# Kernel optimization log

Measured on AMD Instinct MI355X. Metric: run time of the kernel, lower is better.

The kernel has to match this reference:

```python
import jax, jax.numpy as jnp
import numpy as np

B, N, H, HD = 2, 512, 1024, 512


def setup_inputs() -> dict:
    key = jax.random.key(0)
    ks = jax.random.split(key, 9)
    s = 0.02
    return {
        "emb": jax.random.normal(ks[0], (B, N, H), jnp.float32),
        # start detector: Linear(H->HD), ReLU, Linear(HD->1)
        "W_s1": jax.random.normal(ks[1], (H, HD), jnp.float32) * s,
        "b_s1": jax.random.normal(ks[2], (HD,), jnp.float32) * s,
        "w_s2": jax.random.normal(ks[3], (HD,), jnp.float32) * s,
        "b_s2": jax.random.normal(ks[4], (), jnp.float32) * s,
        # end detector: Linear(2H->HD), ReLU, Linear(HD->1)
        "W_e1": jax.random.normal(ks[5], (2 * H, HD), jnp.float32) * s,
        "b_e1": jax.random.normal(ks[6], (HD,), jnp.float32) * s,
        "w_e2": jax.random.normal(ks[7], (HD,), jnp.float32) * s,
        "b_e2": jax.random.normal(ks[8], (), jnp.float32) * s,
    }


def reference(emb, W_s1, b_s1, w_s2, b_s2, W_e1, b_e1, w_e2, b_e2):
    # start logits: (B, N)
    h_s = jax.nn.relu(jnp.einsum("bnh,hd->bnd", emb, W_s1) + b_s1)
    start_logits = jnp.einsum("bnd,d->bn", h_s, w_s2) + b_s2

    # end logits: math of cat([start_rep, end_rep]) @ W_e1 done as split matmuls
    # (avoids materializing the (B,N,N,2H) concat buffer)
    W1_start, W1_end = W_e1[:H], W_e1[H:]
    a = jnp.einsum("bih,hd->bid", emb, W1_start)  # (B, N, HD) start-token part
    c = jnp.einsum("bjh,hd->bjd", emb, W1_end)    # (B, N, HD) end-token part
    h_e = jax.nn.relu(a[:, :, None, :] + c[:, None, :, :] + b_e1)  # (B, N, N, HD)
    end_logits = jnp.einsum("bijd,d->bij", h_e, w_e2) + b_e2       # (B, N, N)

    return (start_logits, end_logits)
```

## Files before the change

### kernel.cpp

```cpp
#include <hip/hip_runtime.h>
#include <hip/hip_bf16.h>


typedef float f32x4 __attribute__((ext_vector_type(4)));
typedef float f32x2 __attribute__((ext_vector_type(2)));
typedef __bf16 bf16x8 __attribute__((ext_vector_type(8)));

static __device__ __forceinline__ unsigned short f2bf(float f) {
  unsigned int u = __builtin_bit_cast(unsigned int, f);
  u += 0x7FFFu + ((u >> 16) & 1u);
  return (unsigned short)(u >> 16);
}

__global__ __launch_bounds__(256) void prep(
    const float* __restrict__ emb, const float* __restrict__ W_s1,
    const float* __restrict__ W_e1, const float* __restrict__ b_s2,
    unsigned short* __restrict__ emb_bf, unsigned short* __restrict__ Wt_s,
    unsigned short* __restrict__ Wt_e, float* __restrict__ out) {
  __shared__ float tile[32][33];
  int bx = blockIdx.x, t = threadIdx.x;
  if (bx < 512) {
    int i = bx * 2048 + t * 8;
    f32x4 v0 = *(const f32x4*)&emb[i];
    f32x4 v1 = *(const f32x4*)&emb[i + 4];
    ushort4 o0, o1;
    o0.x = f2bf(v0[0]); o0.y = f2bf(v0[1]);
    o0.z = f2bf(v0[2]); o0.w = f2bf(v0[3]);
    o1.x = f2bf(v1[0]); o1.y = f2bf(v1[1]);
    o1.z = f2bf(v1[2]); o1.w = f2bf(v1[3]);
    *(ushort4*)&emb_bf[i] = o0;
    *(ushort4*)&emb_bf[i + 4] = o1;
  } else if (bx < 2048) {
    const float* in;
    unsigned short* o;
    int R, tid;
    if (bx < 1024) { tid = bx - 512;  in = W_s1; o = Wt_s; R = 1024; }
    else           { tid = bx - 1024; in = W_e1; o = Wt_e; R = 2048; }
    int r0 = (tid >> 4) * 32, c0 = (tid & 15) * 32;
    int a = t >> 3, b4 = t & 7;
    f32x4 v = *(const f32x4*)&in[(size_t)(r0 + a) * 512 + c0 + b4 * 4];
    tile[a][b4 * 4 + 0] = v[0];
    tile[a][b4 * 4 + 1] = v[1];
    tile[a][b4 * 4 + 2] = v[2];
    tile[a][b4 * 4 + 3] = v[3];
    __syncthreads();
    ushort4 o4;
    o4.x = f2bf(tile[b4 * 4 + 0][a]);
    o4.y = f2bf(tile[b4 * 4 + 1][a]);
    o4.z = f2bf(tile[b4 * 4 + 2][a]);
    o4.w = f2bf(tile[b4 * 4 + 3][a]);
    *(ushort4*)&o[(size_t)(c0 + a) * R + r0 + b4 * 4] = o4;
  } else {
    float v = b_s2[0];
    f32x4 o = {v, v, v, v};
    *(f32x4*)&out[t * 4] = o;
  }
}

__global__ __launch_bounds__(256) void gemm_fused(
    const unsigned short* __restrict__ Aemb,
    const unsigned short* __restrict__ Wt_s,
    const unsigned short* __restrict__ Wt_e,
    const float* __restrict__ b_s1, const float* __restrict__ w_s2,
    const float* __restrict__ b_e1, float* __restrict__ out,
    float* __restrict__ A_mat, float* __restrict__ C_mat) {
  __shared__ unsigned short Al[64][72];
  __shared__ unsigned short Bl[32][72];
  int z = blockIdx.z;
  int n0 = blockIdx.x * 32;
  int m0 = blockIdx.y * 64;
  const unsigned short* Bmat = (z == 0) ? Wt_s : Wt_e;
  int bstride = (z == 0) ? 1024 : 2048;
  int bofs = (z == 2) ? 1024 : 0;

  int t = threadIdx.x, lane = t & 63, wave = t >> 6;
  int wm = wave * 16;
  int lm = lane & 15, g = lane >> 4;

  f32x4 acc[2];
  acc[0] = (f32x4){0.f, 0.f, 0.f, 0.f};
  acc[1] = (f32x4){0.f, 0.f, 0.f, 0.f};

  int ar = t >> 2, ac = (t & 3) * 16;
  int br = t >> 3, bc = (t & 7) * 8;
  for (int k0 = 0; k0 < 1024; k0 += 64) {
    __syncthreads();
    const unsigned short* ap = &Aemb[(size_t)(m0 + ar) * 1024 + k0 + ac];
    *(uint4*)&Al[ar][ac] = *(const uint4*)ap;
    *(uint4*)&Al[ar][ac + 8] = *(const uint4*)(ap + 8);
    *(uint4*)&Bl[br][bc] =
        *(const uint4*)&Bmat[(size_t)(n0 + br) * bstride + bofs + k0 + bc];
    __syncthreads();
#pragma unroll
    for (int kk = 0; kk < 2; ++kk) {
      bf16x8 af = *(const bf16x8*)&Al[wm + lm][kk * 32 + g * 8];
      bf16x8 b0 = *(const bf16x8*)&Bl[lm][kk * 32 + g * 8];
      bf16x8 b1 = *(const bf16x8*)&Bl[16 + lm][kk * 32 + g * 8];
      acc[0] = __builtin_amdgcn_mfma_f32_16x16x32_bf16(af, b0, acc[0], 0, 0, 0);
      acc[1] = __builtin_amdgcn_mfma_f32_16x16x32_bf16(af, b1, acc[1], 0, 0, 0);
    }
  }

  int col0 = n0 + lm, col1 = n0 + 16 + lm;
  if (z == 0) {
    float bs0 = b_s1[col0], bs1 = b_s1[col1];
    float ws0 = w_s2[col0], ws1 = w_s2[col1];
#pragma unroll
    for (int r = 0; r < 4; ++r) {
      float s = fmaxf(acc[0][r] + bs0, 0.f) * ws0 +
                fmaxf(acc[1][r] + bs1, 0.f) * ws1;
      s += __shfl_xor(s, 1);
      s += __shfl_xor(s, 2);
      s += __shfl_xor(s, 4);
      s += __shfl_xor(s, 8);
      if (lm == 0) atomicAdd(&out[m0 + wm + g * 4 + r], s);
    }
  } else {
    float* Out = (z == 1) ? A_mat : C_mat;
    float b0 = (z == 2) ? b_e1[col0] : 0.f;
    float b1 = (z == 2) ? b_e1[col1] : 0.f;
#pragma unroll
    for (int r = 0; r < 4; ++r) {
      int row = m0 + wm + g * 4 + r;
      Out[(size_t)row * 512 + col0] = acc[0][r] + b0;
      Out[(size_t)row * 512 + col1] = acc[1][r] + b1;
    }
  }
}

__global__ __launch_bounds__(512) void pairwise(
    const float* __restrict__ A_mat, const float* __restrict__ C_mat,
    const float* __restrict__ w_e2, const float* __restrict__ b_e2,
    float* __restrict__ out) {
  __shared__ f32x2 As_p[32][32];
  __shared__ f32x2 Cs_p[32][64];
  __shared__ f32x2 wl2[256];
  int t = threadIdx.x;
  int b = blockIdx.z;
  int j0 = blockIdx.x * 64, i0 = blockIdx.y * 32;

  if (t < 256) wl2[t] = *(const f32x2*)&w_e2[2 * t];
  float be2 = b_e2[0];

  int ti = t >> 5, tj = t & 31;
  f32x2 acc2[2][2];
#pragma unroll
  for (int q = 0; q < 2; ++q)
#pragma unroll
    for (int r = 0; r < 2; ++r) acc2[q][r] = (f32x2){0.f, 0.f};

  const float* Ab = A_mat + (size_t)(b * 512 + i0) * 512;
  const float* Cb = C_mat + (size_t)(b * 512 + j0) * 512;
  int si = t & 31, sq = t >> 5;
  int sj = t & 63, s2 = t >> 6;
  f32x2 z2 = {0.f, 0.f};

  for (int ch = 0; ch < 8; ++ch) {
    __syncthreads();
    {
      f32x4 va = *(const f32x4*)&Ab[(size_t)si * 512 + ch * 64 + sq * 4];
      As_p[sq * 2 + 0][si] = (f32x2){va[0], va[1]};
      As_p[sq * 2 + 1][si] = (f32x2){va[2], va[3]};
      f32x4 v0 = *(const f32x4*)&Cb[(size_t)sj * 512 + ch * 64 + s2 * 8];
      f32x4 v1 = *(const f32x4*)&Cb[(size_t)sj * 512 + ch * 64 + s2 * 8 + 4];
      Cs_p[s2 * 4 + 0][sj] = (f32x2){v0[0], v0[1]};
      Cs_p[s2 * 4 + 1][sj] = (f32x2){v0[2], v0[3]};
      Cs_p[s2 * 4 + 2][sj] = (f32x2){v1[0], v1[1]};
      Cs_p[s2 * 4 + 3][sj] = (f32x2){v1[2], v1[3]};
    }
    __syncthreads();
#pragma unroll 8
    for (int dp = 0; dp < 32; ++dp) {
      f32x2 w2 = wl2[ch * 32 + dp];
      f32x4 av = *(const f32x4*)&As_p[dp][ti * 2];
      f32x4 cv = *(const f32x4*)&Cs_p[dp][tj * 2];
      f32x2 a0 = {av[0], av[1]}, a1 = {av[2], av[3]};
      f32x2 c0 = {cv[0], cv[1]}, c1 = {cv[2], cv[3]};
      acc2[0][0] += __builtin_elementwise_max(a0 + c0, z2) * w2;
      acc2[0][1] += __builtin_elementwise_max(a0 + c1, z2) * w2;
      acc2[1][0] += __builtin_elementwise_max(a1 + c0, z2) * w2;
      acc2[1][1] += __builtin_elementwise_max(a1 + c1, z2) * w2;
    }
  }

  float* oe = out + 1024;
#pragma unroll
  for (int q = 0; q < 2; ++q) {
    int i = i0 + ti * 2 + q;
    float2 vv;
    vv.x = acc2[q][0][0] + acc2[q][0][1] + be2;
    vv.y = acc2[q][1][0] + acc2[q][1][1] + be2;
    *(float2*)&oe[(size_t)(b * 512 + i) * 512 + j0 + tj * 2] = vv;
  }
}

extern "C" void kernel_launch(void* const* d_in, const int* in_sizes, int n_in,
                              void* d_out, int out_size, void* d_ws,
                              size_t ws_size, hipStream_t stream) {
  const float* emb  = (const float*)d_in[0];
  const float* W_s1 = (const float*)d_in[1];
  const float* b_s1 = (const float*)d_in[2];
  const float* w_s2 = (const float*)d_in[3];
  const float* b_s2 = (const float*)d_in[4];
  const float* W_e1 = (const float*)d_in[5];
  const float* b_e1 = (const float*)d_in[6];
  const float* w_e2 = (const float*)d_in[7];
  const float* b_e2 = (const float*)d_in[8];
  float* out = (float*)d_out;

  char* ws = (char*)d_ws;
  unsigned short* emb_bf = (unsigned short*)(ws);
  unsigned short* Wt_s = (unsigned short*)(ws + 2u * (1u << 20));
  unsigned short* Wt_e = (unsigned short*)(ws + 3u * (1u << 20));
  float* A_mat = (float*)(ws + 5u * (1u << 20));
  float* C_mat = (float*)(ws + 7u * (1u << 20));

  hipLaunchKernelGGL(prep, dim3(2049), dim3(256), 0, stream,
                     emb, W_s1, W_e1, b_s2, emb_bf, Wt_s, Wt_e, out);
  hipLaunchKernelGGL(gemm_fused, dim3(16, 16, 3), dim3(256), 0, stream,
                     emb_bf, Wt_s, Wt_e, b_s1, w_s2, b_e1, out, A_mat, C_mat);
  hipLaunchKernelGGL(pairwise, dim3(8, 16, 2), dim3(512), 0, stream,
                     A_mat, C_mat, w_e2, b_e2, out);
}
```

Before: 119.0 us.

## Store end-token projection in bf16 and give GEMM waves 2x2 MFMA tiles

The end-token projection C (with its bias) is now written as bf16 instead of fp32. The pairwise kernel stages it as packed bf16 pairs in shared memory and unpacks with shifts and masks, which halves C's global and LDS traffic. Separately, the GEMM now uses 128 threads per block, and each wave computes a 32x32 tile with a 2x2 MFMA register block, so fragments are reused more and fewer waves load the same tiles. The cost is extra rounding error in C and fewer waves per block to hide latency in the GEMM.

```diff
diff --git a/kernel.cpp b/kernel.cpp
--- a/kernel.cpp
+++ b/kernel.cpp
@@ -57,13 +57,13 @@
   }
 }
 
-__global__ __launch_bounds__(256) void gemm_fused(
+__global__ __launch_bounds__(128) void gemm_fused(
     const unsigned short* __restrict__ Aemb,
     const unsigned short* __restrict__ Wt_s,
     const unsigned short* __restrict__ Wt_e,
     const float* __restrict__ b_s1, const float* __restrict__ w_s2,
     const float* __restrict__ b_e1, float* __restrict__ out,
-    float* __restrict__ A_mat, float* __restrict__ C_mat) {
+    float* __restrict__ A_mat, unsigned short* __restrict__ C_bf) {
   __shared__ unsigned short Al[64][72];
   __shared__ unsigned short Bl[32][72];
   int z = blockIdx.z;
@@ -74,30 +74,44 @@
   int bofs = (z == 2) ? 1024 : 0;
 
   int t = threadIdx.x, lane = t & 63, wave = t >> 6;
-  int wm = wave * 16;
+  int wm = wave * 32;
   int lm = lane & 15, g = lane >> 4;
 
-  f32x4 acc[2];
-  acc[0] = (f32x4){0.f, 0.f, 0.f, 0.f};
-  acc[1] = (f32x4){0.f, 0.f, 0.f, 0.f};
-
-  int ar = t >> 2, ac = (t & 3) * 16;
-  int br = t >> 3, bc = (t & 7) * 8;
+  f32x4 acc[2][2];
+#pragma unroll
+  for (int mi = 0; mi < 2; ++mi)
+#pragma unroll
+    for (int ni = 0; ni < 2; ++ni) acc[mi][ni] = (f32x4){0.f, 0.f, 0.f, 0.f};
+
+  int ar = t >> 1, ah = (t & 1) * 32;
+  int br = t >> 2, bs = (t & 3) * 16;
   for (int k0 = 0; k0 < 1024; k0 += 64) {
     __syncthreads();
-    const unsigned short* ap = &Aemb[(size_t)(m0 + ar) * 1024 + k0 + ac];
-    *(uint4*)&Al[ar][ac] = *(const uint4*)ap;
-    *(uint4*)&Al[ar][ac + 8] = *(const uint4*)(ap + 8);
-    *(uint4*)&Bl[br][bc] =
-        *(const uint4*)&Bmat[(size_t)(n0 + br) * bstride + bofs + k0 + bc];
+    const unsigned short* ap = &Aemb[(size_t)(m0 + ar) * 1024 + k0 + ah];
+    *(uint4*)&Al[ar][ah + 0]  = *(const uint4*)(ap + 0);
+    *(uint4*)&Al[ar][ah + 8]  = *(const uint4*)(ap + 8);
+    *(uint4*)&Al[ar][ah + 16] = *(const uint4*)(ap + 16);
+    *(uint4*)&Al[ar][ah + 24] = *(const uint4*)(ap + 24);
+    const unsigned short* bp =
+        &Bmat[(size_t)(n0 + br) * bstride + bofs + k0 + bs];
+    *(uint4*)&Bl[br][bs + 0] = *(const uint4*)(bp + 0);
+    *(uint4*)&Bl[br][bs + 8] = *(const uint4*)(bp + 8);
     __syncthreads();
 #pragma unroll
     for (int kk = 0; kk < 2; ++kk) {
-      bf16x8 af = *(const bf16x8*)&Al[wm + lm][kk * 32 + g * 8];
-      bf16x8 b0 = *(const bf16x8*)&Bl[lm][kk * 32 + g * 8];
-      bf16x8 b1 = *(const bf16x8*)&Bl[16 + lm][kk * 32 + g * 8];
-      acc[0] = __builtin_amdgcn_mfma_f32_16x16x32_bf16(af, b0, acc[0], 0, 0, 0);
-      acc[1] = __builtin_amdgcn_mfma_f32_16x16x32_bf16(af, b1, acc[1], 0, 0, 0);
+      bf16x8 af[2], bf[2];
+#pragma unroll
+      for (int mi = 0; mi < 2; ++mi)
+        af[mi] = *(const bf16x8*)&Al[wm + mi * 16 + lm][kk * 32 + g * 8];
+#pragma unroll
+      for (int ni = 0; ni < 2; ++ni)
+        bf[ni] = *(const bf16x8*)&Bl[ni * 16 + lm][kk * 32 + g * 8];
+#pragma unroll
+      for (int mi = 0; mi < 2; ++mi)
+#pragma unroll
+        for (int ni = 0; ni < 2; ++ni)
+          acc[mi][ni] = __builtin_amdgcn_mfma_f32_16x16x32_bf16(
+              af[mi], bf[ni], acc[mi][ni], 0, 0, 0);
     }
   }
 
@@ -106,34 +120,45 @@
     float bs0 = b_s1[col0], bs1 = b_s1[col1];
     float ws0 = w_s2[col0], ws1 = w_s2[col1];
 #pragma unroll
-    for (int r = 0; r < 4; ++r) {
-      float s = fmaxf(acc[0][r] + bs0, 0.f) * ws0 +
-                fmaxf(acc[1][r] + bs1, 0.f) * ws1;
-      s += __shfl_xor(s, 1);
-      s += __shfl_xor(s, 2);
-      s += __shfl_xor(s, 4);
-      s += __shfl_xor(s, 8);
-      if (lm == 0) atomicAdd(&out[m0 + wm + g * 4 + r], s);
-    }
+    for (int mi = 0; mi < 2; ++mi)
+#pragma unroll
+      for (int r = 0; r < 4; ++r) {
+        float s = fmaxf(acc[mi][0][r] + bs0, 0.f) * ws0 +
+                  fmaxf(acc[mi][1][r] + bs1, 0.f) * ws1;
+        s += __shfl_xor(s, 1);
+        s += __shfl_xor(s, 2);
+        s += __shfl_xor(s, 4);
+        s += __shfl_xor(s, 8);
+        if (lm == 0) atomicAdd(&out[m0 + wm + mi * 16 + g * 4 + r], s);
+      }
+  } else if (z == 1) {
+#pragma unroll
+    for (int mi = 0; mi < 2; ++mi)
+#pragma unroll
+      for (int r = 0; r < 4; ++r) {
+        int row = m0 + wm + mi * 16 + g * 4 + r;
+        A_mat[(size_t)row * 512 + col0] = acc[mi][0][r];
+        A_mat[(size_t)row * 512 + col1] = acc[mi][1][r];
+      }
   } else {
-    float* Out = (z == 1) ? A_mat : C_mat;
-    float b0 = (z == 2) ? b_e1[col0] : 0.f;
-    float b1 = (z == 2) ? b_e1[col1] : 0.f;
-#pragma unroll
-    for (int r = 0; r < 4; ++r) {
-      int row = m0 + wm + g * 4 + r;
-      Out[(size_t)row * 512 + col0] = acc[0][r] + b0;
-      Out[(size_t)row * 512 + col1] = acc[1][r] + b1;
-    }
+    float b0 = b_e1[col0], b1 = b_e1[col1];
+#pragma unroll
+    for (int mi = 0; mi < 2; ++mi)
+#pragma unroll
+      for (int r = 0; r < 4; ++r) {
+        int row = m0 + wm + mi * 16 + g * 4 + r;
+        C_bf[(size_t)row * 512 + col0] = f2bf(acc[mi][0][r] + b0);
+        C_bf[(size_t)row * 512 + col1] = f2bf(acc[mi][1][r] + b1);
+      }
   }
 }
 
 __global__ __launch_bounds__(512) void pairwise(
-    const float* __restrict__ A_mat, const float* __restrict__ C_mat,
+    const float* __restrict__ A_mat, const unsigned short* __restrict__ C_bf,
     const float* __restrict__ w_e2, const float* __restrict__ b_e2,
     float* __restrict__ out) {
   __shared__ f32x2 As_p[32][32];
-  __shared__ f32x2 Cs_p[32][64];
+  __shared__ unsigned int Cs_b[32][64];
   __shared__ f32x2 wl2[256];
   int t = threadIdx.x;
   int b = blockIdx.z;
@@ -150,7 +175,7 @@
     for (int r = 0; r < 2; ++r) acc2[q][r] = (f32x2){0.f, 0.f};
 
   const float* Ab = A_mat + (size_t)(b * 512 + i0) * 512;
-  const float* Cb = C_mat + (size_t)(b * 512 + j0) * 512;
+  const unsigned short* Cb = C_bf + (size_t)(b * 512 + j0) * 512;
   int si = t & 31, sq = t >> 5;
   int sj = t & 63, s2 = t >> 6;
   f32x2 z2 = {0.f, 0.f};
@@ -161,21 +186,23 @@
       f32x4 va = *(const f32x4*)&Ab[(size_t)si * 512 + ch * 64 + sq * 4];
       As_p[sq * 2 + 0][si] = (f32x2){va[0], va[1]};
       As_p[sq * 2 + 1][si] = (f32x2){va[2], va[3]};
-      f32x4 v0 = *(const f32x4*)&Cb[(size_t)sj * 512 + ch * 64 + s2 * 8];
-      f32x4 v1 = *(const f32x4*)&Cb[(size_t)sj * 512 + ch * 64 + s2 * 8 + 4];
-      Cs_p[s2 * 4 + 0][sj] = (f32x2){v0[0], v0[1]};
-      Cs_p[s2 * 4 + 1][sj] = (f32x2){v0[2], v0[3]};
-      Cs_p[s2 * 4 + 2][sj] = (f32x2){v1[0], v1[1]};
-      Cs_p[s2 * 4 + 3][sj] = (f32x2){v1[2], v1[3]};
+      uint4 vc = *(const uint4*)&Cb[(size_t)sj * 512 + ch * 64 + s2 * 8];
+      Cs_b[s2 * 4 + 0][sj] = vc.x;
+      Cs_b[s2 * 4 + 1][sj] = vc.y;
+      Cs_b[s2 * 4 + 2][sj] = vc.z;
+      Cs_b[s2 * 4 + 3][sj] = vc.w;
     }
     __syncthreads();
 #pragma unroll 8
     for (int dp = 0; dp < 32; ++dp) {
       f32x2 w2 = wl2[ch * 32 + dp];
       f32x4 av = *(const f32x4*)&As_p[dp][ti * 2];
-      f32x4 cv = *(const f32x4*)&Cs_p[dp][tj * 2];
+      uint2 cu = *(const uint2*)&Cs_b[dp][tj * 2];
       f32x2 a0 = {av[0], av[1]}, a1 = {av[2], av[3]};
-      f32x2 c0 = {cv[0], cv[1]}, c1 = {cv[2], cv[3]};
+      f32x2 c0 = {__builtin_bit_cast(float, cu.x << 16),
+                  __builtin_bit_cast(float, cu.x & 0xFFFF0000u)};
+      f32x2 c1 = {__builtin_bit_cast(float, cu.y << 16),
+                  __builtin_bit_cast(float, cu.y & 0xFFFF0000u)};
       acc2[0][0] += __builtin_elementwise_max(a0 + c0, z2) * w2;
       acc2[0][1] += __builtin_elementwise_max(a0 + c1, z2) * w2;
       acc2[1][0] += __builtin_elementwise_max(a1 + c0, z2) * w2;
@@ -213,12 +240,12 @@
   unsigned short* Wt_s = (unsigned short*)(ws + 2u * (1u << 20));
   unsigned short* Wt_e = (unsigned short*)(ws + 3u * (1u << 20));
   float* A_mat = (float*)(ws + 5u * (1u << 20));
-  float* C_mat = (float*)(ws + 7u * (1u << 20));
+  unsigned short* C_bf = (unsigned short*)(ws + 7u * (1u << 20));
 
   hipLaunchKernelGGL(prep, dim3(2049), dim3(256), 0, stream,
                      emb, W_s1, W_e1, b_s2, emb_bf, Wt_s, Wt_e, out);
-  hipLaunchKernelGGL(gemm_fused, dim3(16, 16, 3), dim3(256), 0, stream,
-                     emb_bf, Wt_s, Wt_e, b_s1, w_s2, b_e1, out, A_mat, C_mat);
+  hipLaunchKernelGGL(gemm_fused, dim3(16, 16, 3), dim3(128), 0, stream,
+                     emb_bf, Wt_s, Wt_e, b_s1, w_s2, b_e1, out, A_mat, C_bf);
   hipLaunchKernelGGL(pairwise, dim3(8, 16, 2), dim3(512), 0, stream,
-                     A_mat, C_mat, w_e2, b_e2, out);
-}
+                     A_mat, C_bf, w_e2, b_e2, out);
+}
```

After: 131.9 us. 10.8% more time.
